# Performance work log

Hardware: AMD Instinct MI355X
Metric: run time of the kernel (lower is better)

Reference implementation:

```python
import jax, jax.numpy as jnp
import numpy as np

INT4_QMAX = 7.0  # symmetric int4: representable range clipped to [-8, 7]


def simulate_quantize_int4(w):
    # axis_to_reduce=None -> single global scale over the whole kernel
    scale = jnp.max(jnp.abs(w)) / INT4_QMAX
    q = jnp.clip(jnp.round(w / scale), -8.0, 7.0)
    return q * scale


def setup_inputs() -> dict:
    key = jax.random.key(0)
    k_x, k_w, k_bias, k_a, k_b = jax.random.split(key, 5)
    d_in, features, rank = 1024, 1024, 16
    x = jax.random.normal(k_x, (4, 8192, d_in), dtype=jnp.float32)
    kernel = jax.random.normal(k_w, (d_in, features), dtype=jnp.float32)
    bias = jax.random.normal(k_bias, (features,), dtype=jnp.float32)
    a = jax.random.normal(k_a, (d_in, rank), dtype=jnp.float32) * (1.0 / np.sqrt(d_in))
    b = jax.random.normal(k_b, (rank, features), dtype=jnp.float32) * 0.01
    return {"x": x, "kernel": kernel, "bias": bias, "a": a, "b": b}


def reference(x, kernel, bias, a, b):
    # fake-quantized main matmul: y = x @ dequant(quant(W)) + bias
    w = simulate_quantize_int4(kernel)
    y = jnp.einsum('bsd,df->bsf', x, w) + bias
    # LoRA adapter: x @ a @ b (contract small rank dim first)
    lora = jnp.einsum('bsr,rf->bsf', jnp.einsum('bsd,dr->bsr', x, a), b)
    return y + lora
```

## Files before the change

### kernel.cpp

```cpp
#include <hip/hip_runtime.h>
#include <hip/hip_bf16.h>

typedef __bf16 bf16x8 __attribute__((ext_vector_type(8)));
typedef __bf16 bf16x4 __attribute__((ext_vector_type(4)));
typedef float  f32x4  __attribute__((ext_vector_type(4)));

#define K_DIM 1024
#define N_DIM 1024
#define BM 128
#define BN 128
#define BK 64
#define BM2 256
#define BN2 256
#define BK2 32
#define NT2 (K_DIM / BK2)
#define AS_T (BM2 * BK2)
#define BS_T (BN2 * BK2)

typedef unsigned int u32;
typedef u32 __attribute__((address_space(1))) u32_g;
typedef u32 __attribute__((address_space(3))) u32_s;

__device__ __forceinline__ void load16_lds(const void* g, void* s) {
    __builtin_amdgcn_global_load_lds((u32_g*)g, (u32_s*)s, 16, 0, 0);
}

__global__ void maxabs_kernel(const float* __restrict__ w, float* __restrict__ blockmax, int n4) {
    __shared__ float sm[4];
    int i = blockIdx.x * blockDim.x + threadIdx.x;
    int stride = gridDim.x * blockDim.x;
    float m = 0.f;
    for (; i < n4; i += stride) {
        float4 v = ((const float4*)w)[i];
        m = fmaxf(m, fmaxf(fmaxf(fabsf(v.x), fabsf(v.y)), fmaxf(fabsf(v.z), fabsf(v.w))));
    }
#pragma unroll
    for (int off = 32; off > 0; off >>= 1)
        m = fmaxf(m, __shfl_down(m, off, 64));
    int lane = threadIdx.x & 63, wave = threadIdx.x >> 6;
    if (lane == 0) sm[wave] = m;
    __syncthreads();
    if (threadIdx.x == 0)
        blockmax[blockIdx.x] = fmaxf(fmaxf(sm[0], sm[1]), fmaxf(sm[2], sm[3]));
}

__global__ void build_w_kernel(const float* __restrict__ kern, const float* __restrict__ amat,
                               const float* __restrict__ bmat, const float* __restrict__ blockmax,
                               __bf16* __restrict__ wt) {
    __shared__ float smax;
    if (threadIdx.x < 64) {
        float m = 0.f;
#pragma unroll
        for (int j = 0; j < 4; ++j) m = fmaxf(m, blockmax[threadIdx.x + j * 64]);
#pragma unroll
        for (int off = 32; off > 0; off >>= 1)
            m = fmaxf(m, __shfl_down(m, off, 64));
        if (threadIdx.x == 0) smax = m;
    }
    __syncthreads();
    float scale = smax * (1.0f / 7.0f);

    int t = blockIdx.x * blockDim.x + threadIdx.x;
    int k = t & (K_DIM - 1);
    int n = t >> 10;
    float w = kern[k * N_DIM + n];
    float q = rintf(w / scale);
    q = fminf(fmaxf(q, -8.f), 7.f);
    float acc = q * scale;
#pragma unroll
    for (int r = 0; r < 16; ++r)
        acc += amat[k * 16 + r] * bmat[r * N_DIM + n];
    wt[(size_t)n * K_DIM + k] = (__bf16)acc;
}

__global__ void cvt_x_kernel(const float4* __restrict__ x, bf16x8* __restrict__ xb, int n8) {
    int i = blockIdx.x * blockDim.x + threadIdx.x;
    if (i >= n8) return;
    float4 v0 = x[i * 2];
    float4 v1 = x[i * 2 + 1];
    bf16x8 o;
    o[0] = (__bf16)v0.x; o[1] = (__bf16)v0.y; o[2] = (__bf16)v0.z; o[3] = (__bf16)v0.w;
    o[4] = (__bf16)v1.x; o[5] = (__bf16)v1.y; o[6] = (__bf16)v1.z; o[7] = (__bf16)v1.w;
    xb[i] = o;
}

__global__ __launch_bounds__(512, 2)
void gemm256_kernel(const __bf16* __restrict__ xb, const __bf16* __restrict__ wt,
                    const float* __restrict__ bias, float* __restrict__ out) {
    __shared__ __attribute__((aligned(16))) __bf16 As[4][AS_T];
    __shared__ __attribute__((aligned(16))) __bf16 Bs[4][BS_T];

    const int tid  = threadIdx.x;
    const int lane = tid & 63;
    const int wave = tid >> 6;
    const int wr   = wave >> 2;
    const int wc   = wave & 3;
    const int l15  = lane & 15;
    const int l4   = lane >> 4;

    const int lb  = blockIdx.x;
    const int ib  = lb >> 3;
    const int bn0 = (ib & 3) * BN2;
    const int bm0 = (((ib >> 2) << 3) | (lb & 7)) * BM2;

    const int srow = lane >> 2;
    const int lc   = (lane & 3) ^ ((srow >> 1) & 3);

    const __bf16* xg = xb + (size_t)(bm0 + wave * 32 + srow) * K_DIM + lc * 8;
    const __bf16* wg = wt + (size_t)(bn0 + wave * 32 + srow) * K_DIM + lc * 8;
    __bf16* sa = &As[0][wave * 32 * BK2];
    __bf16* sb = &Bs[0][wave * 32 * BK2];

    const int ro = l15 * BK2 + ((l4 ^ ((l15 >> 1) & 3)) << 3);

    f32x4 acc[8][4] = {};

#define STAGE_A(T) do { int b_ = (T) & 3; int k_ = ((T) & 31) * BK2;        \
        load16_lds(xg + k_,              sa + b_ * AS_T);                   \
        load16_lds(xg + 16 * K_DIM + k_, sa + b_ * AS_T + 16 * BK2); } while (0)
#define STAGE_B(T) do { int b_ = (T) & 3; int k_ = ((T) & 31) * BK2;        \
        load16_lds(wg + k_,              sb + b_ * BS_T);                   \
        load16_lds(wg + 16 * K_DIM + k_, sb + b_ * BS_T + 16 * BK2); } while (0)

#define HALF(BUFI, ST) do {                                                  \
        const int buf_ = (BUFI);                                             \
        const __bf16* ap = (const __bf16*)As + buf_ * AS_T + wr * (128 * BK2) + ro; \
        const __bf16* bp = (const __bf16*)Bs + buf_ * BS_T + wc * (64 * BK2) + ro;  \
        bf16x8 af[8], bv[4];                                                 \
        af[0] = *(const bf16x8*)(ap + 0 * (16 * BK2));                       \
        af[1] = *(const bf16x8*)(ap + 1 * (16 * BK2));                       \
        af[2] = *(const bf16x8*)(ap + 2 * (16 * BK2));                       \
        af[3] = *(const bf16x8*)(ap + 3 * (16 * BK2));                       \
        bv[0] = *(const bf16x8*)(bp + 0 * (16 * BK2));                       \
        bv[1] = *(const bf16x8*)(bp + 1 * (16 * BK2));                       \
        af[4] = *(const bf16x8*)(ap + 4 * (16 * BK2));                       \
        af[5] = *(const bf16x8*)(ap + 5 * (16 * BK2));                       \
        af[6] = *(const bf16x8*)(ap + 6 * (16 * BK2));                       \
        af[7] = *(const bf16x8*)(ap + 7 * (16 * BK2));                       \
        bv[2] = *(const bf16x8*)(bp + 2 * (16 * BK2));                       \
        bv[3] = *(const bf16x8*)(bp + 3 * (16 * BK2));                       \
        STAGE_A(ST);                                                         \
        asm volatile("s_waitcnt lgkmcnt(6)" ::: "memory");                   \
        __builtin_amdgcn_sched_barrier(0);                                   \
        __builtin_amdgcn_s_setprio(1);                                       \
        _Pragma("unroll") for (int mt = 0; mt < 4; ++mt)                     \
        _Pragma("unroll") for (int nt = 0; nt < 2; ++nt)                     \
            acc[mt][nt] = __builtin_amdgcn_mfma_f32_16x16x32_bf16(           \
                af[mt], bv[nt], acc[mt][nt], 0, 0, 0);                       \
        asm volatile("s_waitcnt lgkmcnt(2)" ::: "memory");                   \
        __builtin_amdgcn_sched_barrier(0);                                   \
        _Pragma("unroll") for (int mt = 4; mt < 8; ++mt)                     \
        _Pragma("unroll") for (int nt = 0; nt < 2; ++nt)                     \
            acc[mt][nt] = __builtin_amdgcn_mfma_f32_16x16x32_bf16(           \
                af[mt], bv[nt], acc[mt][nt], 0, 0, 0);                       \
        STAGE_B(ST);                                                         \
        asm volatile("s_waitcnt lgkmcnt(0)" ::: "memory");                   \
        __builtin_amdgcn_sched_barrier(0);                                   \
        _Pragma("unroll") for (int mt = 0; mt < 8; ++mt)                     \
        _Pragma("unroll") for (int nt = 2; nt < 4; ++nt)                     \
            acc[mt][nt] = __builtin_amdgcn_mfma_f32_16x16x32_bf16(           \
                af[mt], bv[nt], acc[mt][nt], 0, 0, 0);                       \
        __builtin_amdgcn_s_setprio(0);                                       \
        asm volatile("s_waitcnt vmcnt(8)" ::: "memory");                     \
        __builtin_amdgcn_s_barrier();                                        \
    } while (0)

    STAGE_A(0); STAGE_B(0);
    STAGE_A(1); STAGE_B(1);
    STAGE_A(2); STAGE_B(2);
    asm volatile("s_waitcnt vmcnt(8)" ::: "memory");
    __builtin_amdgcn_s_barrier();

#pragma unroll 1
    for (int u = 0; u < NT2 / 2; ++u) {
        const int t0 = 2 * u;
        HALF(t0 & 3, t0 + 3);
        HALF((t0 + 1) & 3, t0 + 4);
    }
#undef HALF
#undef STAGE_A
#undef STAGE_B

#pragma unroll
    for (int nt = 0; nt < 4; ++nt) {
        int n = bn0 + wc * 64 + nt * 16 + l15;
        float bvs = bias[n];
#pragma unroll
        for (int mt = 0; mt < 8; ++mt) {
            int m = bm0 + wr * 128 + mt * 16 + l4 * 4;
            float* op = out + (size_t)m * N_DIM + n;
#pragma unroll
            for (int r = 0; r < 4; ++r)
                op[(size_t)r * N_DIM] = acc[mt][nt][r] + bvs;
        }
    }
}

__global__ __launch_bounds__(256, 4)
void gemm_fb_kernel(const float* __restrict__ x, const __bf16* __restrict__ wt,
                    const float* __restrict__ bias, float* __restrict__ out) {
    __shared__ __attribute__((aligned(16))) __bf16 As[BM * BK];
    __shared__ __attribute__((aligned(16))) __bf16 Bs[BN * BK];

    const int tid  = threadIdx.x;
    const int lane = tid & 63;
    const int wave = tid >> 6;
    const int wm = (wave >> 1) * 64;
    const int wn = (wave & 1) * 64;

    const int l = blockIdx.x;
    const int i = l >> 3;
    const int bn0 = (i & 7) * BN;
    const int bm0 = (((i >> 3) << 3) | (l & 7)) * BM;

    const int l15 = lane & 15;
    const int l4  = lane >> 4;

    f32x4 acc[4][4] = {};

    const int srow = lane >> 3;
    const int gch  = (lane & 7) ^ srow;

    for (int k0 = 0; k0 < K_DIM; k0 += BK) {
        __syncthreads();
#pragma unroll
        for (int j = 0; j < 4; ++j) {
            int r = j * 32 + wave * 8;
            const __bf16* g = wt + (size_t)(bn0 + r + srow) * K_DIM + k0 + gch * 8;
            load16_lds(g, &Bs[r * BK]);
        }
#pragma unroll
        for (int j = 0; j < 8; ++j) {
            int f  = j * 256 + tid;
            int r  = f >> 4;
            int c4 = f & 15;
            float4 v = *(const float4*)(x + (size_t)(bm0 + r) * K_DIM + k0 + c4 * 4);
            int p = (c4 >> 1) ^ (r & 7);
            bf16x4 o;
            o.x = (__bf16)v.x; o.y = (__bf16)v.y; o.z = (__bf16)v.z; o.w = (__bf16)v.w;
            *(bf16x4*)(&As[r * BK + p * 8 + (c4 & 1) * 4]) = o;
        }
        __syncthreads();

#pragma unroll
        for (int ks = 0; ks < 2; ++ks) {
            bf16x8 af[4], bfr[4];
#pragma unroll
            for (int mt = 0; mt < 4; ++mt) {
                int r = wm + mt * 16 + l15;
                int p = (ks * 4 + l4) ^ (r & 7);
                af[mt] = *(const bf16x8*)(&As[r * BK + p * 8]);
            }
#pragma unroll
            for (int nt = 0; nt < 4; ++nt) {
                int r = wn + nt * 16 + l15;
                int p = (ks * 4 + l4) ^ (r & 7);
                bfr[nt] = *(const bf16x8*)(&Bs[r * BK + p * 8]);
            }
#pragma unroll
            for (int mt = 0; mt < 4; ++mt)
#pragma unroll
                for (int nt = 0; nt < 4; ++nt)
                    acc[mt][nt] = __builtin_amdgcn_mfma_f32_16x16x32_bf16(
                        af[mt], bfr[nt], acc[mt][nt], 0, 0, 0);
        }
    }

#pragma unroll
    for (int nt = 0; nt < 4; ++nt) {
        int n = bn0 + wn + nt * 16 + l15;
        float bv = bias[n];
#pragma unroll
        for (int mt = 0; mt < 4; ++mt) {
            int m = bm0 + wm + mt * 16 + l4 * 4;
            float* op = out + (size_t)m * N_DIM + n;
#pragma unroll
            for (int r = 0; r < 4; ++r)
                op[(size_t)r * N_DIM] = acc[mt][nt][r] + bv;
        }
    }
}

extern "C" void kernel_launch(void* const* d_in, const int* in_sizes, int n_in,
                              void* d_out, int out_size, void* d_ws, size_t ws_size,
                              hipStream_t stream) {
    const float* x    = (const float*)d_in[0];
    const float* kern = (const float*)d_in[1];
    const float* bias = (const float*)d_in[2];
    const float* amat = (const float*)d_in[3];
    const float* bmat = (const float*)d_in[4];
    float* out = (float*)d_out;
    const int M = in_sizes[0] / K_DIM;

    float* blockmax = (float*)d_ws;
    __bf16* wt = (__bf16*)((char*)d_ws + 4096);
    const size_t xb_off    = 4096 + (size_t)N_DIM * K_DIM * sizeof(__bf16);
    const size_t need_fast = xb_off + (size_t)M * K_DIM * sizeof(__bf16);

    maxabs_kernel<<<256, 256, 0, stream>>>(kern, blockmax, K_DIM * N_DIM / 4);
    build_w_kernel<<<K_DIM * N_DIM / 256, 256, 0, stream>>>(kern, amat, bmat, blockmax, wt);

    if (ws_size >= need_fast && (M % (BM2 * 8)) == 0) {
        __bf16* xbuf = (__bf16*)((char*)d_ws + xb_off);
        int n8 = M * K_DIM / 8;
        cvt_x_kernel<<<(n8 + 255) / 256, 256, 0, stream>>>((const float4*)x, (bf16x8*)xbuf, n8);
        gemm256_kernel<<<(M / BM2) * (N_DIM / BN2), 512, 0, stream>>>(xbuf, wt, bias, out);
    } else {
        gemm_fb_kernel<<<(M / BM) * (N_DIM / BN), 256, 0, stream>>>(x, wt, bias, out);
    }
}
```

Before: 317.2 us.

## Fuse fp32-to-bf16 conversion of x into GEMM via register-staged A loads

Removes the separate x conversion kernel and its bf16 workspace buffer; the GEMM now loads fp32 x into registers, converts to bf16, and writes into a double-buffered LDS tile. B keeps its async global-to-LDS 4-stage pipeline while A is prefetched two iterations ahead in registers. This eliminates a full extra read/write pass over the activation, at the cost of higher fp32 read traffic per tile, more VGPRs, and VALU conversion work inside the main loop.

After: 309.2 us. 2.5% less time.

```diff
diff --git a/kernel.cpp b/kernel.cpp
--- a/kernel.cpp
+++ b/kernel.cpp
@@ -73,21 +73,10 @@
     wt[(size_t)n * K_DIM + k] = (__bf16)acc;
 }
 
-__global__ void cvt_x_kernel(const float4* __restrict__ x, bf16x8* __restrict__ xb, int n8) {
-    int i = blockIdx.x * blockDim.x + threadIdx.x;
-    if (i >= n8) return;
-    float4 v0 = x[i * 2];
-    float4 v1 = x[i * 2 + 1];
-    bf16x8 o;
-    o[0] = (__bf16)v0.x; o[1] = (__bf16)v0.y; o[2] = (__bf16)v0.z; o[3] = (__bf16)v0.w;
-    o[4] = (__bf16)v1.x; o[5] = (__bf16)v1.y; o[6] = (__bf16)v1.z; o[7] = (__bf16)v1.w;
-    xb[i] = o;
-}
-
 __global__ __launch_bounds__(512, 2)
-void gemm256_kernel(const __bf16* __restrict__ xb, const __bf16* __restrict__ wt,
+void gemm256_kernel(const float* __restrict__ x, const __bf16* __restrict__ wt,
                     const float* __restrict__ bias, float* __restrict__ out) {
-    __shared__ __attribute__((aligned(16))) __bf16 As[4][AS_T];
+    __shared__ __attribute__((aligned(16))) __bf16 As[2][AS_T];
     __shared__ __attribute__((aligned(16))) __bf16 Bs[4][BS_T];
 
     const int tid  = threadIdx.x;
@@ -105,27 +94,53 @@
 
     const int srow = lane >> 2;
     const int lc   = (lane & 3) ^ ((srow >> 1) & 3);
-
-    const __bf16* xg = xb + (size_t)(bm0 + wave * 32 + srow) * K_DIM + lc * 8;
     const __bf16* wg = wt + (size_t)(bn0 + wave * 32 + srow) * K_DIM + lc * 8;
-    __bf16* sa = &As[0][wave * 32 * BK2];
     __bf16* sb = &Bs[0][wave * 32 * BK2];
 
+    const int r0  = tid >> 3;
+    const int c4  = tid & 7;
+    const int apc = (c4 >> 1) ^ ((r0 >> 1) & 3);
+    const int awr = r0 * BK2 + apc * 8 + (c4 & 1) * 4;
+    const float* ag = x + (size_t)(bm0 + r0) * K_DIM + c4 * 4;
+
     const int ro = l15 * BK2 + ((l4 ^ ((l15 >> 1) & 3)) << 3);
 
     f32x4 acc[8][4] = {};
-
-#define STAGE_A(T) do { int b_ = (T) & 3; int k_ = ((T) & 31) * BK2;        \
-        load16_lds(xg + k_,              sa + b_ * AS_T);                   \
-        load16_lds(xg + 16 * K_DIM + k_, sa + b_ * AS_T + 16 * BK2); } while (0)
+    float4 av0, av1, av2, av3;
+
 #define STAGE_B(T) do { int b_ = (T) & 3; int k_ = ((T) & 31) * BK2;        \
         load16_lds(wg + k_,              sb + b_ * BS_T);                   \
         load16_lds(wg + 16 * K_DIM + k_, sb + b_ * BS_T + 16 * BK2); } while (0)
 
-#define HALF(BUFI, ST) do {                                                  \
-        const int buf_ = (BUFI);                                             \
+#define LOADA(T) do { const float* p_ = ag + ((T) & 31) * BK2;              \
+        av0 = *(const float4*)(p_);                                         \
+        av1 = *(const float4*)(p_ +  64 * K_DIM);                           \
+        av2 = *(const float4*)(p_ + 128 * K_DIM);                           \
+        av3 = *(const float4*)(p_ + 192 * K_DIM); } while (0)
+
+#define WRITEA(T) do { __bf16* d_ = &As[(T) & 1][awr];                      \
+        bf16x4 o0, o1, o2, o3;                                              \
+        o0.x=(__bf16)av0.x; o0.y=(__bf16)av0.y; o0.z=(__bf16)av0.z; o0.w=(__bf16)av0.w; \
+        o1.x=(__bf16)av1.x; o1.y=(__bf16)av1.y; o1.z=(__bf16)av1.z; o1.w=(__bf16)av1.w; \
+        o2.x=(__bf16)av2.x; o2.y=(__bf16)av2.y; o2.z=(__bf16)av2.z; o2.w=(__bf16)av2.w; \
+        o3.x=(__bf16)av3.x; o3.y=(__bf16)av3.y; o3.z=(__bf16)av3.z; o3.w=(__bf16)av3.w; \
+        *(bf16x4*)(d_)        = o0;  *(bf16x4*)(d_ + 2048) = o1;            \
+        *(bf16x4*)(d_ + 4096) = o2;  *(bf16x4*)(d_ + 6144) = o3; } while (0)
+
+    LOADA(0);
+    STAGE_B(0); STAGE_B(1); STAGE_B(2);
+    asm volatile("s_waitcnt vmcnt(6)" ::: "memory");
+    __builtin_amdgcn_sched_barrier(0);
+    WRITEA(0);
+    LOADA(1);
+    asm volatile("s_waitcnt vmcnt(8)" ::: "memory");
+    asm volatile("s_waitcnt lgkmcnt(0)" ::: "memory");
+    __builtin_amdgcn_s_barrier();
+
+#define ITER(t) do {                                                         \
+        const int buf_ = (t) & 1; const int bbuf_ = (t) & 3;                 \
         const __bf16* ap = (const __bf16*)As + buf_ * AS_T + wr * (128 * BK2) + ro; \
-        const __bf16* bp = (const __bf16*)Bs + buf_ * BS_T + wc * (64 * BK2) + ro;  \
+        const __bf16* bp = (const __bf16*)Bs + bbuf_ * BS_T + wc * (64 * BK2) + ro; \
         bf16x8 af[8], bv[4];                                                 \
         af[0] = *(const bf16x8*)(ap + 0 * (16 * BK2));                       \
         af[1] = *(const bf16x8*)(ap + 1 * (16 * BK2));                       \
@@ -139,7 +154,7 @@
         af[7] = *(const bf16x8*)(ap + 7 * (16 * BK2));                       \
         bv[2] = *(const bf16x8*)(bp + 2 * (16 * BK2));                       \
         bv[3] = *(const bf16x8*)(bp + 3 * (16 * BK2));                       \
-        STAGE_A(ST);                                                         \
+        STAGE_B((t) + 3);                                                    \
         asm volatile("s_waitcnt lgkmcnt(6)" ::: "memory");                   \
         __builtin_amdgcn_sched_barrier(0);                                   \
         __builtin_amdgcn_s_setprio(1);                                       \
@@ -153,7 +168,10 @@
         _Pragma("unroll") for (int nt = 0; nt < 2; ++nt)                     \
             acc[mt][nt] = __builtin_amdgcn_mfma_f32_16x16x32_bf16(           \
                 af[mt], bv[nt], acc[mt][nt], 0, 0, 0);                       \
-        STAGE_B(ST);                                                         \
+        asm volatile("s_waitcnt vmcnt(2)" ::: "memory");                     \
+        __builtin_amdgcn_sched_barrier(0);                                   \
+        WRITEA((t) + 1);                                                     \
+        LOADA((t) + 2);                                                      \
         asm volatile("s_waitcnt lgkmcnt(0)" ::: "memory");                   \
         __builtin_amdgcn_sched_barrier(0);                                   \
         _Pragma("unroll") for (int mt = 0; mt < 8; ++mt)                     \
@@ -161,25 +179,15 @@
             acc[mt][nt] = __builtin_amdgcn_mfma_f32_16x16x32_bf16(           \
                 af[mt], bv[nt], acc[mt][nt], 0, 0, 0);                       \
         __builtin_amdgcn_s_setprio(0);                                       \
-        asm volatile("s_waitcnt vmcnt(8)" ::: "memory");                     \
         __builtin_amdgcn_s_barrier();                                        \
     } while (0)
 
-    STAGE_A(0); STAGE_B(0);
-    STAGE_A(1); STAGE_B(1);
-    STAGE_A(2); STAGE_B(2);
-    asm volatile("s_waitcnt vmcnt(8)" ::: "memory");
-    __builtin_amdgcn_s_barrier();
-
-#pragma unroll 1
-    for (int u = 0; u < NT2 / 2; ++u) {
-        const int t0 = 2 * u;
-        HALF(t0 & 3, t0 + 3);
-        HALF((t0 + 1) & 3, t0 + 4);
-    }
-#undef HALF
-#undef STAGE_A
+#pragma unroll 4
+    for (int t = 0; t < NT2; ++t) ITER(t);
+#undef ITER
 #undef STAGE_B
+#undef LOADA
+#undef WRITEA
 
 #pragma unroll
     for (int nt = 0; nt < 4; ++nt) {
@@ -294,17 +302,14 @@
 
     float* blockmax = (float*)d_ws;
     __bf16* wt = (__bf16*)((char*)d_ws + 4096);
-    const size_t xb_off    = 4096 + (size_t)N_DIM * K_DIM * sizeof(__bf16);
-    const size_t need_fast = xb_off + (size_t)M * K_DIM * sizeof(__bf16);
+    const size_t need = 4096 + (size_t)N_DIM * K_DIM * sizeof(__bf16);
+    (void)need;
 
     maxabs_kernel<<<256, 256, 0, stream>>>(kern, blockmax, K_DIM * N_DIM / 4);
     build_w_kernel<<<K_DIM * N_DIM / 256, 256, 0, stream>>>(kern, amat, bmat, blockmax, wt);
 
-    if (ws_size >= need_fast && (M % (BM2 * 8)) == 0) {
-        __bf16* xbuf = (__bf16*)((char*)d_ws + xb_off);
-        int n8 = M * K_DIM / 8;
-        cvt_x_kernel<<<(n8 + 255) / 256, 256, 0, stream>>>((const float4*)x, (bf16x8*)xbuf, n8);
-        gemm256_kernel<<<(M / BM2) * (N_DIM / BN2), 512, 0, stream>>>(xbuf, wt, bias, out);
+    if ((M % (BM2 * 8)) == 0) {
+        gemm256_kernel<<<(M / BM2) * (N_DIM / BN2), 512, 0, stream>>>(x, wt, bias, out);
     } else {
         gemm_fb_kernel<<<(M / BM) * (N_DIM / BN), 256, 0, stream>>>(x, wt, bias, out);
     }
```
